# Kernel tuning notes

Hardware: AMD Instinct MI355X
Metric: run time of the kernel (lower is better)

## Reference

```python
import jax, jax.numpy as jnp
import numpy as np

N = 100000
E = 1600000
EVENT_DIM = 64
HID = 128


def setup_inputs() -> dict:
    key = jax.random.key(0)
    ks = jax.random.split(key, 12)
    def lin(kw, kb, fan_in, fan_out):
        bound = 1.0 / np.sqrt(fan_in)
        W = jax.random.uniform(kw, (fan_in, fan_out), jnp.float32, -bound, bound)
        b = jax.random.uniform(kb, (fan_out,), jnp.float32, -bound, bound)
        return W, b
    base_feat = jax.random.normal(ks[0], (N, HID), jnp.float32)
    event_vector = jax.random.normal(ks[1], (N, EVENT_DIM), jnp.float32)
    edge_index = jax.random.randint(ks[2], (2, E), 0, N, jnp.int64)
    W_proj, b_proj = lin(ks[3], ks[4], EVENT_DIM, HID)
    W_gcn, b_gcn = lin(ks[5], ks[6], HID, HID)
    W_gate, b_gate = lin(ks[7], ks[8], 2 * HID, HID)
    W_fuse, b_fuse = lin(ks[9], ks[10], 2 * HID, HID)
    return {"base_feat": base_feat, "event_vector": event_vector,
            "edge_index": edge_index,
            "W_proj": W_proj, "b_proj": b_proj,
            "W_gcn": W_gcn, "b_gcn": b_gcn,
            "W_gate": W_gate, "b_gate": b_gate,
            "W_fuse": W_fuse, "b_fuse": b_fuse}


def gcn_conv(x, edge_index, W, b, n):
    # PyG GCNConv: x @ W, add self-loops, symmetric deg^-1/2 normalization,
    # scatter-sum into target nodes, then + bias.
    x = x @ W  # [N, H]
    loop = jnp.arange(n, dtype=edge_index.dtype)
    src = jnp.concatenate([edge_index[0], loop])
    dst = jnp.concatenate([edge_index[1], loop])
    deg = jax.ops.segment_sum(jnp.ones_like(dst, dtype=x.dtype), dst, num_segments=n)
    dis = jnp.where(deg > 0, jax.lax.rsqrt(deg), 0.0)
    norm = dis[src] * dis[dst]  # [E+N]
    msgs = x[src] * norm[:, None]  # gather + scale
    out = jax.ops.segment_sum(msgs, dst, num_segments=n)  # scatter-sum
    return out + b


def reference(base_feat, event_vector, edge_index,
              W_proj, b_proj, W_gcn, b_gcn, W_gate, b_gate, W_fuse, b_fuse):
    n = base_feat.shape[0]
    event_feat = jax.nn.relu(event_vector @ W_proj + b_proj)
    diffused = jax.nn.relu(gcn_conv(event_feat, edge_index, W_gcn, b_gcn, n))
    gate_in = jnp.concatenate([base_feat, diffused], axis=-1)
    gate = jax.nn.sigmoid(gate_in @ W_gate + b_gate)
    corrected = base_feat * (1.0 - gate) + diffused * gate
    fuse_in = jnp.concatenate([base_feat, corrected], axis=-1)
    return jax.nn.relu(fuse_in @ W_fuse + b_fuse)
```

## Files before the change

kernel.cpp:

```cpp
#include <hip/hip_runtime.h>


typedef unsigned short inj_u16;
typedef unsigned int   inj_u32;
typedef __attribute__((ext_vector_type(8))) short bf16x8;
typedef __attribute__((ext_vector_type(4))) float f32x4;

static constexpr int INJ_N  = 100000;
static constexpr int INJ_E  = 1600000;
static constexpr int INJ_H  = 128;
static constexpr int INJ_D  = 64;
static constexpr int INJ_NB = 196;
static constexpr int INJ_CH = 6400;
static constexpr int INJ_PB = 250;

__device__ __forceinline__ float inj_b2f(inj_u16 h){
  union { inj_u32 u; float f; } c; c.u = ((inj_u32)h) << 16; return c.f;
}
__device__ __forceinline__ inj_u16 inj_f2b(float x){
  union { inj_u32 u; float f; } c; c.f = x;
  return (inj_u16)((c.u + 0x7FFFu + ((c.u >> 16) & 1u)) >> 16);
}
__device__ __forceinline__ float inj_lo(inj_u32 w){ return inj_b2f((inj_u16)(w & 0xFFFFu)); }
__device__ __forceinline__ float inj_hi(inj_u32 w){ return inj_b2f((inj_u16)(w >> 16)); }
__device__ __forceinline__ inj_u32 inj_pack(float a, float b){
  return ((inj_u32)inj_f2b(b) << 16) | (inj_u32)inj_f2b(a);
}
__device__ __forceinline__ float inj_ld1(const void* p, size_t i, int f32){
  return f32 ? ((const float*)p)[i] : inj_b2f(((const inj_u16*)p)[i]);
}
__device__ __forceinline__ float2 inj_ld2(const void* p, size_t pair, int f32){
  if (f32) return ((const float2*)p)[pair];
  inj_u32 w = ((const inj_u32*)p)[pair];
  float2 r; r.x = inj_lo(w); r.y = inj_hi(w);
  return r;
}

__global__ void inj_flags(const int* eidx, const inj_u32* base, int* flags){
  int l = threadIdx.x & 63;
  unsigned long long nz = __ballot(eidx[2*l + 1] != 0);
  inj_u32 ex = (base[l] >> 7) & 0xFFu;
  unsigned long long inr = __ballot(ex >= 100u && ex <= 135u);
  if (threadIdx.x == 0){
    flags[0] = (nz == 0ull) ? 1 : 0;
    flags[1] = (__popcll(inr) >= 56) ? 0 : 1;
  }
}

__device__ __forceinline__ int inj_eread(const int* e, size_t i, int w64){
  return w64 ? e[2*i] : e[i];
}

__global__ __launch_bounds__(256) void inj_bhist(const int* eidx, int* bhp,
                                                 const int* flags){
  __shared__ int h[INJ_NB];
  const int tid = threadIdx.x;
  const int e0 = blockIdx.x * INJ_CH;
  const int w64 = flags[0];
  for (int b = tid; b < INJ_NB; b += 256) h[b] = 0;
  __syncthreads();
  for (int i = tid; i < INJ_CH; i += 256){
    int dst = inj_eread(eidx, (size_t)INJ_E + e0 + i, w64);
    atomicAdd(&h[dst >> 9], 1);
  }
  __syncthreads();
  for (int b = tid; b < INJ_NB; b += 256)
    if (h[b]) atomicAdd(&bhp[b*16], h[b]);
}

__global__ void inj_bscan(const int* bhp, int* bbase, int* bcurA, int* rowp){
  __shared__ int s[256];
  int tid = threadIdx.x;
  int v = (tid < INJ_NB) ? bhp[tid*16] : 0;
  s[tid] = v; __syncthreads();
  for (int off = 1; off < 256; off <<= 1){
    int t = (tid >= off) ? s[tid - off] : 0;
    __syncthreads();
    s[tid] += t;
    __syncthreads();
  }
  if (tid < INJ_NB){
    int base = s[tid] - v;
    bbase[tid]    = base;
    bcurA[tid*16] = base;
  }
  if (tid == 0){ bbase[INJ_NB] = INJ_E; rowp[INJ_N] = INJ_E; }
}

__global__ __launch_bounds__(256) void inj_passA(
    const int* eidx, int* bcurA, inj_u32* pairs, const int* flags){
  __shared__ inj_u32 sedge[INJ_CH];
  __shared__ unsigned char sbkt[INJ_CH];
  __shared__ int scnt[INJ_NB];
  __shared__ int scur[INJ_NB];
  const int tid = threadIdx.x;
  const int e0 = blockIdx.x * INJ_CH;
  const int w64 = flags[0];
  for (int b = tid; b < INJ_NB; b += 256) scnt[b] = 0;
  __syncthreads();
  for (int i = tid; i < INJ_CH; i += 256){
    int src = inj_eread(eidx, (size_t)(e0 + i), w64);
    int dst = inj_eread(eidx, (size_t)INJ_E + e0 + i, w64);
    int b = dst >> 9;
    sedge[i] = (inj_u32)src | ((inj_u32)(dst & 511) << 17);
    sbkt[i] = (unsigned char)b;
    atomicAdd(&scnt[b], 1);
  }
  __syncthreads();
  for (int b = tid; b < INJ_NB; b += 256){
    int c = scnt[b];
    scur[b] = c ? atomicAdd(&bcurA[b*16], c) : 0;
  }
  __syncthreads();
  for (int i = tid; i < INJ_CH; i += 256){
    int b = sbkt[i];
    int pos = atomicAdd(&scur[b], 1);
    pairs[pos] = sedge[i];
  }
}

__global__ __launch_bounds__(256) void inj_passB(
    const inj_u32* pairs, const int* bbase, int* rowp, float* dis, int* es){
  __shared__ int lcnt[512];
  __shared__ int lcur[512];
  __shared__ int ls[512];
  __shared__ int ws[256];
  const int b = blockIdx.x, tid = threadIdx.x;
  const int beg = bbase[b], endp = bbase[b+1];
  const int nbase = b << 9;
  const int nn = min(512, INJ_N - nbase);
  for (int i = tid; i < 512; i += 256) lcnt[i] = 0;
  __syncthreads();
  for (int p = beg + tid; p < endp; p += 256)
    atomicAdd(&lcnt[pairs[p] >> 17], 1);
  __syncthreads();
  int v0 = lcnt[2*tid], v1 = lcnt[2*tid + 1];
  int psum = v0 + v1;
  ws[tid] = psum; __syncthreads();
  for (int off = 1; off < 256; off <<= 1){
    int t = (tid >= off) ? ws[tid - off] : 0;
    __syncthreads();
    ws[tid] += t;
    __syncthreads();
  }
  int ex0 = ws[tid] - psum;
  ls[2*tid]     = ex0;
  ls[2*tid + 1] = ex0 + v0;
  __syncthreads();
  for (int i = tid; i < nn; i += 256){
    int ex = beg + ls[i];
    rowp[nbase + i] = ex;
    lcur[i] = ex;
    dis[nbase + i] = rsqrtf((float)(lcnt[i] + 1));
  }
  __syncthreads();
  for (int p = beg + tid; p < endp; p += 256){
    inj_u32 w = pairs[p];
    int pos = atomicAdd(&lcur[w >> 17], 1);
    es[pos] = (int)(w & 0x1FFFFu);
  }
}

__global__ void inj_wfrag(const void* Wgate, const void* Wfuse,
                          const void* Wp, const void* Wg,
                          inj_u16* wfrag, inj_u16* wpf, inj_u16* wgf2,
                          const int* flags){
  int t = blockIdx.x*256 + threadIdx.x;
  int f32 = flags[1];
  const void* W; inj_u16* dst; int kbase, n;
  if (t < 8192){
    int mat = t >> 12, r = t & 4095;
    int ct = r >> 9, kk = (r >> 6) & 7, lane = r & 63;
    W = mat ? Wfuse : Wgate;
    dst = wfrag + (size_t)mat*32768 + ((ct*8 + kk)*64 + lane)*8;
    kbase = kk*32 + (lane>>4)*8;
    n = ct*16 + (lane & 15);
  } else if (t < 9216){
    int r = t - 8192;
    int ct = r >> 7, kk = (r >> 6) & 1, lane = r & 63;
    W = Wp;
    dst = wpf + ((ct*2 + kk)*64 + lane)*8;
    kbase = kk*32 + (lane>>4)*8;
    n = ct*16 + (lane & 15);
  } else {
    int r = t - 9216;
    int ct = r >> 8, kk = (r >> 6) & 3, lane = r & 63;
    W = Wg;
    dst = wgf2 + ((ct*4 + kk)*64 + lane)*8;
    kbase = kk*32 + (lane>>4)*8;
    n = ct*16 + (lane & 15);
  }
  #pragma unroll
  for (int j=0;j<8;j++)
    dst[j] = inj_f2b(inj_ld1(W, (size_t)(kbase + j)*INJ_H + n, f32));
}

__global__ __launch_bounds__(256) void inj_projgcn(
    const void* ev, const void* bp,
    const inj_u16* wpf, const inj_u16* wgf2,
    const float* dis, inj_u32* x, const int* flags){
  __shared__ __align__(16) inj_u16 s_a [ 8*136];
  __shared__ __align__(16) inj_u16 s_ef[16*136];
  __shared__ float s_dis[16];
  const int f32 = flags[1];
  const int tid = threadIdx.x;
  const int n0 = blockIdx.x * 16;

  if (tid < 128){
    int m = tid >> 3, g = tid & 7;
    uint4 v;
    if (!f32){
      v = ((const uint4*)ev)[(size_t)(n0 + m)*8 + g];
    } else {
      const float4* e4 = (const float4*)ev;
      float4 x0 = e4[(size_t)(n0 + m)*16 + g*2];
      float4 x1 = e4[(size_t)(n0 + m)*16 + g*2 + 1];
      v.x = inj_pack(x0.x, x0.y); v.y = inj_pack(x0.z, x0.w);
      v.z = inj_pack(x1.x, x1.y); v.w = inj_pack(x1.z, x1.w);
    }
    *(uint4*)(s_a + g*136 + m*8) = v;
  }
  if (tid < 16) s_dis[tid] = dis[n0 + tid];
  __syncthreads();

  const int lane = tid & 63, wave = tid >> 6;
  const int mrow = lane & 15, quad = lane >> 4;

  float bp0 = inj_ld1(bp, (wave*2    )*16 + mrow, f32);
  float bp1 = inj_ld1(bp, (wave*2 + 1)*16 + mrow, f32);
  f32x4 acc[2] = {{bp0,bp0,bp0,bp0},{bp1,bp1,bp1,bp1}};
  #pragma unroll
  for (int kk = 0; kk < 2; kk++){
    bf16x8 a  = *(const bf16x8*)(s_a + (kk*4 + quad)*136 + mrow*8);
    bf16x8 b0 = *(const bf16x8*)(wpf + (((wave*2    )*2 + kk)*64 + lane)*8);
    bf16x8 b1 = *(const bf16x8*)(wpf + (((wave*2 + 1)*2 + kk)*64 + lane)*8);
    acc[0] = __builtin_amdgcn_mfma_f32_16x16x32_bf16(a, b0, acc[0], 0, 0, 0);
    acc[1] = __builtin_amdgcn_mfma_f32_16x16x32_bf16(a, b1, acc[1], 0, 0, 0);
  }
  #pragma unroll
  for (int t = 0; t < 2; t++){
    int col = (wave*2 + t)*16 + mrow;
    int goff = (col >> 3)*136 + (col & 7);
    #pragma unroll
    for (int r = 0; r < 4; r++){
      int row = quad*4 + r;
      s_ef[goff + row*8] = inj_f2b(fmaxf(acc[t][r], 0.f));
    }
  }
  __syncthreads();

  f32x4 acc2[2] = {{0.f,0.f,0.f,0.f},{0.f,0.f,0.f,0.f}};
  #pragma unroll
  for (int kk = 0; kk < 4; kk++){
    bf16x8 a  = *(const bf16x8*)(s_ef + (kk*4 + quad)*136 + mrow*8);
    bf16x8 b0 = *(const bf16x8*)(wgf2 + (((wave*2    )*4 + kk)*64 + lane)*8);
    bf16x8 b1 = *(const bf16x8*)(wgf2 + (((wave*2 + 1)*4 + kk)*64 + lane)*8);
    acc2[0] = __builtin_amdgcn_mfma_f32_16x16x32_bf16(a, b0, acc2[0], 0, 0, 0);
    acc2[1] = __builtin_amdgcn_mfma_f32_16x16x32_bf16(a, b1, acc2[1], 0, 0, 0);
  }
  inj_u16* xo = (inj_u16*)x;
  #pragma unroll
  for (int t = 0; t < 2; t++){
    int col = (wave*2 + t)*16 + mrow;
    #pragma unroll
    for (int r = 0; r < 4; r++){
      int row = quad*4 + r;
      xo[(size_t)(n0 + row)*INJ_H + col] = inj_f2b(acc2[t][r] * s_dis[row]);
    }
  }
}

__global__ __launch_bounds__(256) void InjectionLayer_91130616086689_kernel(
    const void* base, const void* bgate, const void* bfuse,
    const inj_u16* wgf, const inj_u16* wff,
    const inj_u32* x, const int* rowp, const int* es, const float* dis,
    const void* bgcn, void* outp, const int* flags){
  __shared__ __align__(16) inj_u16 s_b[16*136];
  __shared__ __align__(16) inj_u16 s_d[16*136];
  __shared__ __align__(16) inj_u16 s_c[16*136];
  const int f32 = flags[1];
  const int tid = threadIdx.x;
  const int n0 = blockIdx.x * 16;
  const int lane = tid & 63, wave = tid >> 6;

  {
    int m = tid >> 4, g = tid & 15;
    uint4 vb;
    if (!f32){
      vb = ((const uint4*)base)[(size_t)(n0 + m)*16 + g];
    } else {
      const float4* b4 = (const float4*)base;
      float4 x0 = b4[(size_t)(n0 + m)*32 + g*2];
      float4 x1 = b4[(size_t)(n0 + m)*32 + g*2 + 1];
      vb.x = inj_pack(x0.x, x0.y); vb.y = inj_pack(x0.z, x0.w);
      vb.z = inj_pack(x1.x, x1.y); vb.w = inj_pack(x1.z, x1.w);
    }
    *(uint4*)(s_b + g*136 + m*8) = vb;
  }

  {
    float2 bg = inj_ld2(bgcn, lane, f32);
    const int doff = (lane >> 2)*136 + ((2*lane) & 7);
    for (int t = 0; t < 4; t++){
      const int m = wave*4 + t;
      const int n = n0 + m;
      const float dd = dis[n];
      inj_u32 xv = x[(size_t)n*64 + lane];
      float a0 = inj_lo(xv), a1 = inj_hi(xv);
      const int beg = rowp[n], end = rowp[n+1];
      for (int c = beg; c < end; c += 64){
        int mm = end - c; if (mm > 64) mm = 64;
        int srcv = (lane < mm) ? es[c + lane] : 0;
        int j = 0;
        for (; j + 16 <= mm; j += 16){
          inj_u32 v[16];
          #pragma unroll
          for (int q = 0; q < 16; q++){
            int s = __shfl(srcv, j + q);
            v[q] = x[(size_t)s*64 + lane];
          }
          a0 += (((inj_lo(v[0]) + inj_lo(v[1])) + (inj_lo(v[2]) + inj_lo(v[3])))
               + ((inj_lo(v[4]) + inj_lo(v[5])) + (inj_lo(v[6]) + inj_lo(v[7]))))
              + (((inj_lo(v[8]) + inj_lo(v[9])) + (inj_lo(v[10]) + inj_lo(v[11])))
               + ((inj_lo(v[12]) + inj_lo(v[13])) + (inj_lo(v[14]) + inj_lo(v[15]))));
          a1 += (((inj_hi(v[0]) + inj_hi(v[1])) + (inj_hi(v[2]) + inj_hi(v[3])))
               + ((inj_hi(v[4]) + inj_hi(v[5])) + (inj_hi(v[6]) + inj_hi(v[7]))))
              + (((inj_hi(v[8]) + inj_hi(v[9])) + (inj_hi(v[10]) + inj_hi(v[11])))
               + ((inj_hi(v[12]) + inj_hi(v[13])) + (inj_hi(v[14]) + inj_hi(v[15]))));
        }
        for (; j + 8 <= mm; j += 8){
          inj_u32 v[8];
          #pragma unroll
          for (int q = 0; q < 8; q++){
            int s = __shfl(srcv, j + q);
            v[q] = x[(size_t)s*64 + lane];
          }
          a0 += ((inj_lo(v[0]) + inj_lo(v[1])) + (inj_lo(v[2]) + inj_lo(v[3])))
              + ((inj_lo(v[4]) + inj_lo(v[5])) + (inj_lo(v[6]) + inj_lo(v[7])));
          a1 += ((inj_hi(v[0]) + inj_hi(v[1])) + (inj_hi(v[2]) + inj_hi(v[3])))
              + ((inj_hi(v[4]) + inj_hi(v[5])) + (inj_hi(v[6]) + inj_hi(v[7])));
        }
        for (; j + 4 <= mm; j += 4){
          inj_u32 v[4];
          #pragma unroll
          for (int q = 0; q < 4; q++){
            int s = __shfl(srcv, j + q);
            v[q] = x[(size_t)s*64 + lane];
          }
          a0 += (inj_lo(v[0]) + inj_lo(v[1])) + (inj_lo(v[2]) + inj_lo(v[3]));
          a1 += (inj_hi(v[0]) + inj_hi(v[1])) + (inj_hi(v[2]) + inj_hi(v[3]));
        }
        for (; j < mm; ++j){
          inj_u32 v = x[(size_t)__shfl(srcv, j)*64 + lane];
          a0 += inj_lo(v);
          a1 += inj_hi(v);
        }
      }
      a0 = fmaxf(fmaf(a0, dd, bg.x), 0.f);
      a1 = fmaxf(fmaf(a1, dd, bg.y), 0.f);
      *(inj_u32*)(s_d + doff + m*8) = inj_pack(a0, a1);
    }
  }
  __syncthreads();

  const int mrow = lane & 15, quad = lane >> 4;

  f32x4 accg[2] = {{0.f,0.f,0.f,0.f},{0.f,0.f,0.f,0.f}};
  #pragma unroll
  for (int kk = 0; kk < 8; kk++){
    const inj_u16* mat = (kk < 4) ? s_b : s_d;
    int g = (kk & 3)*4 + quad;
    bf16x8 a = *(const bf16x8*)(mat + g*136 + mrow*8);
    bf16x8 b0 = *(const bf16x8*)(wgf + (((wave*2    )*8 + kk)*64 + lane)*8);
    bf16x8 b1 = *(const bf16x8*)(wgf + (((wave*2 + 1)*8 + kk)*64 + lane)*8);
    accg[0] = __builtin_amdgcn_mfma_f32_16x16x32_bf16(a, b0, accg[0], 0, 0, 0);
    accg[1] = __builtin_amdgcn_mfma_f32_16x16x32_bf16(a, b1, accg[1], 0, 0, 0);
  }

  #pragma unroll
  for (int t = 0; t < 2; t++){
    int col = (wave*2 + t)*16 + mrow;
    float bg = inj_ld1(bgate, col, f32);
    int gk = (col >> 5)*4 + ((col >> 3) & 3), jj = col & 7;
    #pragma unroll
    for (int r = 0; r < 4; r++){
      int row = quad*4 + r;
      float gate = 1.f/(1.f + expf(-(accg[t][r] + bg)));
      int off = gk*136 + row*8 + jj;
      float bb = inj_b2f(s_b[off]);
      float dd = inj_b2f(s_d[off]);
      s_c[off] = inj_f2b(bb*(1.f - gate) + dd*gate);
    }
  }
  __syncthreads();

  f32x4 accf[2] = {{0.f,0.f,0.f,0.f},{0.f,0.f,0.f,0.f}};
  #pragma unroll
  for (int kk = 0; kk < 8; kk++){
    const inj_u16* mat = (kk < 4) ? s_b : s_c;
    int g = (kk & 3)*4 + quad;
    bf16x8 a = *(const bf16x8*)(mat + g*136 + mrow*8);
    bf16x8 b0 = *(const bf16x8*)(wff + (((wave*2    )*8 + kk)*64 + lane)*8);
    bf16x8 b1 = *(const bf16x8*)(wff + (((wave*2 + 1)*8 + kk)*64 + lane)*8);
    accf[0] = __builtin_amdgcn_mfma_f32_16x16x32_bf16(a, b0, accf[0], 0, 0, 0);
    accf[1] = __builtin_amdgcn_mfma_f32_16x16x32_bf16(a, b1, accf[1], 0, 0, 0);
  }
  #pragma unroll
  for (int t = 0; t < 2; t++){
    int col = (wave*2 + t)*16 + mrow;
    float bf = inj_ld1(bfuse, col, f32);
    #pragma unroll
    for (int r = 0; r < 4; r++){
      int row = quad*4 + r;
      float v = fmaxf(accf[t][r] + bf, 0.f);
      size_t oi = (size_t)(n0 + row)*INJ_H + col;
      if (f32) ((float*)outp)[oi] = v;
      else     ((inj_u16*)outp)[oi] = inj_f2b(v);
    }
  }
}

extern "C" __attribute__((visibility("default")))
void kernel_launch(void* const* d_in, const int* in_sizes, int n_in,
                   void* d_out, int out_size, void* d_ws, size_t ws_size,
                   hipStream_t stream) {
  const void* base  = d_in[0];
  const void* ev    = d_in[1];
  const int*  eidx  = (const int*)d_in[2];
  const void* Wp    = d_in[3];
  const void* bp    = d_in[4];
  const void* Wg    = d_in[5];
  const void* bg    = d_in[6];
  const void* Wgate = d_in[7];
  const void* bgate = d_in[8];
  const void* Wfuse = d_in[9];
  const void* bfuse = d_in[10];

  char* ws = (char*)d_ws;
  inj_u32* x      = (inj_u32*)(ws);
  inj_u32* pairs  = (inj_u32*)(ws);
  int*     es     = (int*)    (ws + 25600000);
  int*     bhp    = (int*)    (ws + 32000000);
  inj_u16* wpf    = (inj_u16*)(ws + 32016384);
  inj_u16* wgf2   = (inj_u16*)(ws + 32032768);
  int*     bbase  = (int*)    (ws + 32065536);
  int*     rowp   = (int*)    (ws + 32400000);
  int*     bcurA  = (int*)    (ws + 32800016);
  float*   dis    = (float*)  (ws + 33200016);
  int*     flags  = (int*)    (ws + 33601600);
  inj_u16* wfrag  = (inj_u16*)(ws + 33601664);

  hipMemsetAsync(bhp, 0, (size_t)INJ_NB*64, stream);
  inj_flags  <<<1, 64, 0, stream>>>(eidx, (const inj_u32*)base, flags);
  inj_bhist  <<<INJ_PB, 256, 0, stream>>>(eidx, bhp, flags);
  inj_wfrag  <<<44, 256, 0, stream>>>(Wgate, Wfuse, Wp, Wg, wfrag, wpf, wgf2, flags);
  inj_bscan  <<<1, 256, 0, stream>>>(bhp, bbase, bcurA, rowp);
  inj_passA  <<<INJ_PB, 256, 0, stream>>>(eidx, bcurA, pairs, flags);
  inj_passB  <<<INJ_NB, 256, 0, stream>>>(pairs, bbase, rowp, dis, es);
  inj_projgcn<<<INJ_N/16, 256, 0, stream>>>(ev, bp, wpf, wgf2, dis, x, flags);
  InjectionLayer_91130616086689_kernel<<<INJ_N/16, 256, 0, stream>>>(
      base, bgate, bfuse, wfrag, wfrag + 32768,
      x, rowp, es, dis, bg, d_out, flags);
}
```

Measured before the change: 311.0 us.

## Halve final kernel block to two waves and reuse gate buffer in LDS

The final fused kernel now runs with 128 threads (two waves) per 16-node block instead of four. Each wave aggregates eight nodes instead of four and computes four MFMA column tiles instead of two. The corrected features overwrite s_d in place, which drops one LDS buffer, and an extra barrier guards that overwrite. The 16-wide unrolled gather loop is also removed. Together these aim to shrink per-block resources and raise block residency, at the cost of less latency hiding per block and more serial work per wave in the gather phase.

```diff
diff --git a/kernel.cpp b/kernel.cpp
--- a/kernel.cpp
+++ b/kernel.cpp
@@ -270,21 +270,20 @@
   }
 }
 
-__global__ __launch_bounds__(256) void InjectionLayer_91130616086689_kernel(
+__global__ __launch_bounds__(128) void InjectionLayer_91130616086689_kernel(
     const void* base, const void* bgate, const void* bfuse,
     const inj_u16* wgf, const inj_u16* wff,
     const inj_u32* x, const int* rowp, const int* es, const float* dis,
     const void* bgcn, void* outp, const int* flags){
   __shared__ __align__(16) inj_u16 s_b[16*136];
   __shared__ __align__(16) inj_u16 s_d[16*136];
-  __shared__ __align__(16) inj_u16 s_c[16*136];
   const int f32 = flags[1];
   const int tid = threadIdx.x;
   const int n0 = blockIdx.x * 16;
   const int lane = tid & 63, wave = tid >> 6;
 
-  {
-    int m = tid >> 4, g = tid & 15;
+  for (int i = tid; i < 256; i += 128){
+    int m = i >> 4, g = i & 15;
     uint4 vb;
     if (!f32){
       vb = ((const uint4*)base)[(size_t)(n0 + m)*16 + g];
@@ -301,8 +300,8 @@
   {
     float2 bg = inj_ld2(bgcn, lane, f32);
     const int doff = (lane >> 2)*136 + ((2*lane) & 7);
-    for (int t = 0; t < 4; t++){
-      const int m = wave*4 + t;
+    for (int t = 0; t < 8; t++){
+      const int m = wave*8 + t;
       const int n = n0 + m;
       const float dd = dis[n];
       inj_u32 xv = x[(size_t)n*64 + lane];
@@ -312,22 +311,6 @@
         int mm = end - c; if (mm > 64) mm = 64;
         int srcv = (lane < mm) ? es[c + lane] : 0;
         int j = 0;
-        for (; j + 16 <= mm; j += 16){
-          inj_u32 v[16];
-          #pragma unroll
-          for (int q = 0; q < 16; q++){
-            int s = __shfl(srcv, j + q);
-            v[q] = x[(size_t)s*64 + lane];
-          }
-          a0 += (((inj_lo(v[0]) + inj_lo(v[1])) + (inj_lo(v[2]) + inj_lo(v[3])))
-               + ((inj_lo(v[4]) + inj_lo(v[5])) + (inj_lo(v[6]) + inj_lo(v[7]))))
-              + (((inj_lo(v[8]) + inj_lo(v[9])) + (inj_lo(v[10]) + inj_lo(v[11])))
-               + ((inj_lo(v[12]) + inj_lo(v[13])) + (inj_lo(v[14]) + inj_lo(v[15]))));
-          a1 += (((inj_hi(v[0]) + inj_hi(v[1])) + (inj_hi(v[2]) + inj_hi(v[3])))
-               + ((inj_hi(v[4]) + inj_hi(v[5])) + (inj_hi(v[6]) + inj_hi(v[7]))))
-              + (((inj_hi(v[8]) + inj_hi(v[9])) + (inj_hi(v[10]) + inj_hi(v[11])))
-               + ((inj_hi(v[12]) + inj_hi(v[13])) + (inj_hi(v[14]) + inj_hi(v[15]))));
-        }
         for (; j + 8 <= mm; j += 8){
           inj_u32 v[8];
           #pragma unroll
@@ -365,49 +348,54 @@
 
   const int mrow = lane & 15, quad = lane >> 4;
 
-  f32x4 accg[2] = {{0.f,0.f,0.f,0.f},{0.f,0.f,0.f,0.f}};
+  f32x4 accg[4] = {{0.f,0.f,0.f,0.f},{0.f,0.f,0.f,0.f},
+                   {0.f,0.f,0.f,0.f},{0.f,0.f,0.f,0.f}};
   #pragma unroll
   for (int kk = 0; kk < 8; kk++){
     const inj_u16* mat = (kk < 4) ? s_b : s_d;
     int g = (kk & 3)*4 + quad;
     bf16x8 a = *(const bf16x8*)(mat + g*136 + mrow*8);
-    bf16x8 b0 = *(const bf16x8*)(wgf + (((wave*2    )*8 + kk)*64 + lane)*8);
-    bf16x8 b1 = *(const bf16x8*)(wgf + (((wave*2 + 1)*8 + kk)*64 + lane)*8);
-    accg[0] = __builtin_amdgcn_mfma_f32_16x16x32_bf16(a, b0, accg[0], 0, 0, 0);
-    accg[1] = __builtin_amdgcn_mfma_f32_16x16x32_bf16(a, b1, accg[1], 0, 0, 0);
-  }
-
-  #pragma unroll
-  for (int t = 0; t < 2; t++){
-    int col = (wave*2 + t)*16 + mrow;
-    float bg = inj_ld1(bgate, col, f32);
+    #pragma unroll
+    for (int t = 0; t < 4; t++){
+      bf16x8 b = *(const bf16x8*)(wgf + ((((wave*4 + t)*8 + kk)*64 + lane)*8));
+      accg[t] = __builtin_amdgcn_mfma_f32_16x16x32_bf16(a, b, accg[t], 0, 0, 0);
+    }
+  }
+  __syncthreads();
+
+  #pragma unroll
+  for (int t = 0; t < 4; t++){
+    int col = (wave*4 + t)*16 + mrow;
+    float bgt = inj_ld1(bgate, col, f32);
     int gk = (col >> 5)*4 + ((col >> 3) & 3), jj = col & 7;
     #pragma unroll
     for (int r = 0; r < 4; r++){
       int row = quad*4 + r;
-      float gate = 1.f/(1.f + expf(-(accg[t][r] + bg)));
+      float gate = 1.f/(1.f + expf(-(accg[t][r] + bgt)));
       int off = gk*136 + row*8 + jj;
       float bb = inj_b2f(s_b[off]);
       float dd = inj_b2f(s_d[off]);
-      s_c[off] = inj_f2b(bb*(1.f - gate) + dd*gate);
-    }
-  }
-  __syncthreads();
-
-  f32x4 accf[2] = {{0.f,0.f,0.f,0.f},{0.f,0.f,0.f,0.f}};
+      s_d[off] = inj_f2b(bb*(1.f - gate) + dd*gate);
+    }
+  }
+  __syncthreads();
+
+  f32x4 accf[4] = {{0.f,0.f,0.f,0.f},{0.f,0.f,0.f,0.f},
+                   {0.f,0.f,0.f,0.f},{0.f,0.f,0.f,0.f}};
   #pragma unroll
   for (int kk = 0; kk < 8; kk++){
-    const inj_u16* mat = (kk < 4) ? s_b : s_c;
+    const inj_u16* mat = (kk < 4) ? s_b : s_d;
     int g = (kk & 3)*4 + quad;
     bf16x8 a = *(const bf16x8*)(mat + g*136 + mrow*8);
-    bf16x8 b0 = *(const bf16x8*)(wff + (((wave*2    )*8 + kk)*64 + lane)*8);
-    bf16x8 b1 = *(const bf16x8*)(wff + (((wave*2 + 1)*8 + kk)*64 + lane)*8);
-    accf[0] = __builtin_amdgcn_mfma_f32_16x16x32_bf16(a, b0, accf[0], 0, 0, 0);
-    accf[1] = __builtin_amdgcn_mfma_f32_16x16x32_bf16(a, b1, accf[1], 0, 0, 0);
-  }
-  #pragma unroll
-  for (int t = 0; t < 2; t++){
-    int col = (wave*2 + t)*16 + mrow;
+    #pragma unroll
+    for (int t = 0; t < 4; t++){
+      bf16x8 b = *(const bf16x8*)(wff + ((((wave*4 + t)*8 + kk)*64 + lane)*8));
+      accf[t] = __builtin_amdgcn_mfma_f32_16x16x32_bf16(a, b, accf[t], 0, 0, 0);
+    }
+  }
+  #pragma unroll
+  for (int t = 0; t < 4; t++){
+    int col = (wave*4 + t)*16 + mrow;
     float bf = inj_ld1(bfuse, col, f32);
     #pragma unroll
     for (int r = 0; r < 4; r++){
@@ -458,7 +446,7 @@
   inj_passA  <<<INJ_PB, 256, 0, stream>>>(eidx, bcurA, pairs, flags);
   inj_passB  <<<INJ_NB, 256, 0, stream>>>(pairs, bbase, rowp, dis, es);
   inj_projgcn<<<INJ_N/16, 256, 0, stream>>>(ev, bp, wpf, wgf2, dis, x, flags);
-  InjectionLayer_91130616086689_kernel<<<INJ_N/16, 256, 0, stream>>>(
+  InjectionLayer_91130616086689_kernel<<<INJ_N/16, 128, 0, stream>>>(
       base, bgate, bfuse, wfrag, wfrag + 32768,
       x, rowp, es, dis, bg, d_out, flags);
 }
```

Measured after the change: 319.5 us. +2.7%, slower.
